# Optimization experiments

Hardware: AMD Instinct MI355X
Metric: run time of the kernel (lower is better)

Reference implementation:

```python
import jax, jax.numpy as jnp
import numpy as np

HEADS = 16
DIM_HEAD = 64


def setup_inputs() -> dict:
    key = jax.random.key(0)
    ks = jax.random.split(key, 5)
    b, n, dim = 4, 2048, 1024
    return {
        "x": jax.random.normal(ks[0], (b, n, dim), dtype=jnp.float32),
        "Wq": jax.random.normal(ks[1], (dim, HEADS * DIM_HEAD), dtype=jnp.float32) * (dim ** -0.5),
        "Wkv": jax.random.normal(ks[2], (dim, DIM_HEAD), dtype=jnp.float32) * (dim ** -0.5),
        "null_kv": jax.random.normal(ks[3], (DIM_HEAD,), dtype=jnp.float32),
        "Wout": jax.random.normal(ks[4], (HEADS * DIM_HEAD, dim), dtype=jnp.float32) * ((HEADS * DIM_HEAD) ** -0.5),
    }


def reference(x, Wq, Wkv, null_kv, Wout):
    b, n, dim = x.shape
    scale = DIM_HEAD ** -0.5
    # q: [b, h, n, d], pre-scaled
    q = (x @ Wq).reshape(b, n, HEADS, DIM_HEAD).transpose(0, 2, 1, 3) * scale
    # shared single-head kv: [b, n, d], prepend null token -> [b, n+1, d]
    kv = x @ Wkv
    kv = jnp.concatenate([jnp.broadcast_to(null_kv, (b, 1, DIM_HEAD)), kv], axis=1)
    # sim: [b, h, n, n+1]
    sim = jnp.einsum('bhid,bjd->bhij', q, kv)
    mask_value = -jnp.finfo(sim.dtype).max
    # causal: query i may attend kv cols 0..i+1 (null at col 0)
    i, j = sim.shape[-2], sim.shape[-1]
    causal_mask = jnp.triu(jnp.ones((i, j), dtype=bool), k=j - i + 1)
    sim = jnp.where(causal_mask, mask_value, sim)
    attn = jax.nn.softmax(sim.astype(jnp.float32), axis=-1)
    out = jnp.einsum('bhij,bjd->bhid', attn, kv.astype(jnp.float32))
    out = out.transpose(0, 2, 1, 3).reshape(b, n, HEADS * DIM_HEAD)
    return out @ Wout
```

## Files before the change

### kernel.cpp

```cpp
#include <hip/hip_runtime.h>
#include <hip/hip_bf16.h>

#define HEADS  16
#define DHEAD  64
#define BATCH  4
#define SEQ    2048
#define DIM    1024
#define KVROWS 2112
#define CSHIFT 24.0f

typedef __hip_bfloat16 bf16;
typedef __attribute__((ext_vector_type(8))) short s8v;
typedef __attribute__((ext_vector_type(4))) short s4v;
typedef __attribute__((ext_vector_type(4))) float f4v;

__device__ __forceinline__ void gl_lds16(const void* g, void* l) {
  __builtin_amdgcn_global_load_lds(
      (const __attribute__((address_space(1))) unsigned int*)g,
      (__attribute__((address_space(3))) unsigned int*)l, 16, 0, 0);
}

__global__ void convert_kernel(const float* __restrict__ in, bf16* __restrict__ out) {
  const size_t i = ((size_t)blockIdx.x * 256 + threadIdx.x) * 8;
  const float4 a = *(const float4*)&in[i];
  const float4 b = *(const float4*)&in[i + 4];
  bf16 v[8] = {__float2bfloat16(a.x), __float2bfloat16(a.y),
               __float2bfloat16(a.z), __float2bfloat16(a.w),
               __float2bfloat16(b.x), __float2bfloat16(b.y),
               __float2bfloat16(b.z), __float2bfloat16(b.w)};
  *(s8v*)&out[i] = *(s8v*)v;
}

__global__ void transpose3_kernel(const float* __restrict__ Wq,
                                  const float* __restrict__ Wout,
                                  const float* __restrict__ Wkv,
                                  bf16* __restrict__ WqkvT,
                                  bf16* __restrict__ WoutT) {
  __shared__ bf16 tile[32][33];
  int bid = blockIdx.x;
  const float* src; bf16* dst; int R, C, bx, by;
  if (bid < 1024)      { src = Wq;   dst = WqkvT;                       R = DIM; C = DIM;   bx = bid & 31; by = bid >> 5; }
  else if (bid < 2048) { bid -= 1024; src = Wout; dst = WoutT;          R = DIM; C = DIM;   bx = bid & 31; by = bid >> 5; }
  else                 { bid -= 2048; src = Wkv;  dst = WqkvT + DIM*DIM; R = DIM; C = DHEAD; bx = bid & 1;  by = bid >> 1; }
  const int c0 = bx * 32, r0 = by * 32;
  const int tx = threadIdx.x, ty = threadIdx.y;
#pragma unroll
  for (int i = 0; i < 32; i += 8)
    tile[ty + i][tx] = __float2bfloat16(src[(size_t)(r0 + ty + i) * C + c0 + tx]);
  __syncthreads();
#pragma unroll
  for (int i = 0; i < 32; i += 8)
    dst[(size_t)(c0 + ty + i) * R + r0 + tx] = tile[tx][ty + i];
}

#define GEMM_CORE(A_, BT_, K_)                                                \
  __shared__ bf16 As[2 * 128 * 64];                                           \
  __shared__ bf16 Bs[2 * 128 * 64];                                           \
  const int m0 = blockIdx.x * 128, n0 = blockIdx.y * 128;                     \
  const int t = threadIdx.x;                                                  \
  const int w = t >> 6, l = t & 63, lr = l & 15, lq = l >> 4;                 \
  const int wm = (w & 1) * 64, wn = (w >> 1) * 64;                            \
  f4v acc[4][4] = {};                                                         \
  const int rowl = l >> 2;                                                    \
  const int cl = ((l & 3) ^ ((l >> 3) & 3)) * 8;                              \
  const bf16* gA0 = (A_)  + (size_t)(m0 + 32 * w + rowl) * (K_) + cl;         \
  const bf16* gA1 = (A_)  + (size_t)(m0 + 32 * w + 16 + rowl) * (K_) + cl;    \
  const bf16* gB0 = (BT_) + (size_t)(n0 + 32 * w + rowl) * (K_) + cl;         \
  const bf16* gB1 = (BT_) + (size_t)(n0 + 32 * w + 16 + rowl) * (K_) + cl;    \
  const int sw = lq ^ ((lr >> 1) & 3);                                        \
  STAGEG(0, 0);                                                               \
  __syncthreads();                                                            \
  int cur = 0;                                                                \
  for (int k0 = 0; k0 < (K_); k0 += 64) {                                     \
    if (k0 + 64 < (K_)) STAGEG(cur ^ 1, k0 + 64);                             \
    const s8v* As16 = (const s8v*)(As + cur * 8192);                          \
    const s8v* Bs16 = (const s8v*)(Bs + cur * 8192);                          \
    _Pragma("unroll")                                                         \
    for (int kw = 0; kw < 2; kw++) {                                          \
      s8v a[4], b[4];                                                         \
      _Pragma("unroll")                                                       \
      for (int mt = 0; mt < 4; mt++)                                          \
        a[mt] = As16[kw * 512 + (wm + mt * 16 + lr) * 4 + sw];                \
      _Pragma("unroll")                                                       \
      for (int ct = 0; ct < 4; ct++)                                          \
        b[ct] = Bs16[kw * 512 + (wn + ct * 16 + lr) * 4 + sw];                \
      _Pragma("unroll")                                                       \
      for (int mt = 0; mt < 4; mt++)                                          \
        _Pragma("unroll")                                                     \
        for (int ct = 0; ct < 4; ct++)                                        \
          acc[mt][ct] = __builtin_amdgcn_mfma_f32_16x16x32_bf16(              \
              a[mt], b[ct], acc[mt][ct], 0, 0, 0);                            \
    }                                                                         \
    __syncthreads();                                                          \
    cur ^= 1;                                                                 \
  }

#define STAGEG(bi, kk)                                                        \
  do {                                                                        \
    gl_lds16(gA0 + (kk),      As + (bi) * 8192 + (2 * w) * 512);              \
    gl_lds16(gA1 + (kk),      As + (bi) * 8192 + (2 * w + 1) * 512);          \
    gl_lds16(gB0 + (kk),      Bs + (bi) * 8192 + (2 * w) * 512);              \
    gl_lds16(gB1 + (kk),      Bs + (bi) * 8192 + (2 * w + 1) * 512);          \
    gl_lds16(gA0 + (kk) + 32, As + (bi) * 8192 + 4096 + (2 * w) * 512);       \
    gl_lds16(gA1 + (kk) + 32, As + (bi) * 8192 + 4096 + (2 * w + 1) * 512);   \
    gl_lds16(gB0 + (kk) + 32, Bs + (bi) * 8192 + 4096 + (2 * w) * 512);       \
    gl_lds16(gB1 + (kk) + 32, Bs + (bi) * 8192 + 4096 + (2 * w + 1) * 512);   \
  } while (0)

__global__ __launch_bounds__(256) void gemm_out_kernel(
    const bf16* __restrict__ A, const bf16* __restrict__ BT,
    float* __restrict__ C, int K) {
  GEMM_CORE(A, BT, K)
#pragma unroll
  for (int mt = 0; mt < 4; mt++)
#pragma unroll
    for (int ct = 0; ct < 4; ct++)
#pragma unroll
      for (int r = 0; r < 4; r++) {
        const int row = m0 + wm + mt * 16 + lq * 4 + r;
        const int col = n0 + wn + ct * 16 + lr;
        C[(size_t)row * DIM + col] = acc[mt][ct][r];
      }
}

__global__ __launch_bounds__(256) void gemm_qkv_kernel(
    const bf16* __restrict__ A, const bf16* __restrict__ BT,
    bf16* __restrict__ q, bf16* __restrict__ kvbuf, bf16* __restrict__ kvbufT,
    int K, float alpha) {
  GEMM_CORE(A, BT, K)
  if (blockIdx.y < 8) {
#pragma unroll
    for (int mt = 0; mt < 4; mt++)
#pragma unroll
      for (int ct = 0; ct < 4; ct++)
#pragma unroll
        for (int r = 0; r < 4; r++) {
          const int row = m0 + wm + mt * 16 + lq * 4 + r;
          const int col = n0 + wn + ct * 16 + lr;
          q[(size_t)row * DIM + col] = __float2bfloat16(acc[mt][ct][r] * alpha);
        }
  } else if (wn == 0) {
#pragma unroll
    for (int mt = 0; mt < 4; mt++)
#pragma unroll
      for (int ct = 0; ct < 4; ct++)
#pragma unroll
        for (int r = 0; r < 4; r++) {
          const int m = m0 + wm + mt * 16 + lq * 4 + r;
          const int c = ct * 16 + lr;
          const int bb = m >> 11, jj = (m & 2047) + 1;
          const bf16 v = __float2bfloat16(acc[mt][ct][r]);
          kvbuf [(size_t)(bb * KVROWS + jj) * DHEAD + c] = v;
          kvbufT[(size_t)(bb * DHEAD + c) * KVROWS + jj] = v;
        }
  }
}

__global__ void fill_null_tail_kernel(const float* __restrict__ null_kv,
                                      bf16* __restrict__ kvbuf,
                                      bf16* __restrict__ kvbufT) {
  const int idx = blockIdx.x * 256 + threadIdx.x;
  const int d = idx & 63;
  const int s = (idx >> 6) & 63;
  const int b = idx >> 12;
  const int row = (s == 0) ? 0 : 2048 + s;
  const bf16 v = (s == 0) ? __float2bfloat16(null_kv[d]) : __float2bfloat16(0.f);
  kvbuf [(size_t)(b * KVROWS + row) * DHEAD + d] = v;
  kvbufT[(size_t)(b * DHEAD + d) * KVROWS + row] = v;
}

__global__ __launch_bounds__(256) void attn_kernel(
    const bf16* __restrict__ q,
    const bf16* __restrict__ kv,
    const bf16* __restrict__ kvT,
    bf16* __restrict__ o) {
  __shared__ bf16 kvs [64][68];
  __shared__ bf16 kvsT[64][68];
  __shared__ bf16 Ps[4][16][68];
  const int t = threadIdx.x, w = t >> 6, l = t & 63, lr = l & 15, lq = l >> 4;
  const int blk = blockIdx.x;
  const int qt = 31 - (blk >> 5);
  const int rem = blk & 31, hp = rem >> 2, b = rem & 3;
  const int q0 = qt * 64;
  const int iw = q0 + w * 16 + lr;

  const bf16* qbase = q + ((size_t)(b * SEQ) + iw) * DIM + hp * 128;
  s8v qb[2][2];
#pragma unroll
  for (int hh = 0; hh < 2; hh++) {
    qb[hh][0] = *(const s8v*)&qbase[hh * 64 + lq * 8];
    qb[hh][1] = *(const s8v*)&qbase[hh * 64 + 32 + lq * 8];
  }

  f4v oaccT[2][4] = {};
  float l_lane[2] = {0.f, 0.f};
  const bf16* kvb  = kv  + (size_t)b * KVROWS * DHEAD;
  const bf16* kvTb = kvT + (size_t)b * DHEAD * KVROWS;
  const int jend = q0 + 65;
  const int srow = t >> 2, scol = (t & 3) * 16;

  s8v rkv0 = *(const s8v*)&kvb[(size_t)srow * DHEAD + scol];
  s8v rkv1 = *(const s8v*)&kvb[(size_t)srow * DHEAD + scol + 8];
  s8v rkT0 = *(const s8v*)&kvTb[(size_t)srow * KVROWS + scol];
  s8v rkT1 = *(const s8v*)&kvTb[(size_t)srow * KVROWS + scol + 8];

  for (int j0 = 0; j0 < jend; j0 += 64) {
    __syncthreads();
    *(s8v*)&kvs[srow][scol]      = rkv0;
    *(s8v*)&kvs[srow][scol + 8]  = rkv1;
    *(s8v*)&kvsT[srow][scol]     = rkT0;
    *(s8v*)&kvsT[srow][scol + 8] = rkT1;
    __syncthreads();

    const int jn = min(j0 + 64, KVROWS - 64);
    rkv0 = *(const s8v*)&kvb[(size_t)(jn + srow) * DHEAD + scol];
    rkv1 = *(const s8v*)&kvb[(size_t)(jn + srow) * DHEAD + scol + 8];
    rkT0 = *(const s8v*)&kvTb[(size_t)srow * KVROWS + jn + scol];
    rkT1 = *(const s8v*)&kvTb[(size_t)srow * KVROWS + jn + scol + 8];

    f4v st[2][4];
#pragma unroll
    for (int jt = 0; jt < 4; jt++) {
      s8v a0 = *(const s8v*)&kvs[jt * 16 + lr][lq * 8];
      s8v a1 = *(const s8v*)&kvs[jt * 16 + lr][32 + lq * 8];
#pragma unroll
      for (int hh = 0; hh < 2; hh++) {
        f4v z = {-CSHIFT, -CSHIFT, -CSHIFT, -CSHIFT};
        z = __builtin_amdgcn_mfma_f32_16x16x32_bf16(a0, qb[hh][0], z, 0, 0, 0);
        z = __builtin_amdgcn_mfma_f32_16x16x32_bf16(a1, qb[hh][1], z, 0, 0, 0);
        st[hh][jt] = z;
      }
    }

    const bool diag = (j0 + 62 > q0 + w * 16);
#pragma unroll
    for (int hh = 0; hh < 2; hh++) {
      if (diag) {
#pragma unroll
        for (int jt = 0; jt < 4; jt++)
#pragma unroll
          for (int r = 0; r < 4; r++) {
            const int jg = j0 + jt * 16 + lq * 4 + r;
            if (jg > iw + 1) st[hh][jt][r] = -1e30f;
          }
      }
      float rs = 0.f;
#pragma unroll
      for (int jt = 0; jt < 4; jt++)
#pragma unroll
        for (int r = 0; r < 4; r++) {
          const float pv = exp2f(st[hh][jt][r]);
          st[hh][jt][r] = pv;
          rs += pv;
        }
      l_lane[hh] += rs;

#pragma unroll
      for (int jt = 0; jt < 4; jt++) {
        s4v pk;
#pragma unroll
        for (int r = 0; r < 4; r++) {
          bf16 h16 = __float2bfloat16(st[hh][jt][r]);
          pk[r] = *(short*)&h16;
        }
        *(s4v*)&Ps[w][lr][jt * 16 + lq * 4] = pk;
      }
      const s8v pb0 = *(const s8v*)&Ps[w][lr][lq * 8];
      const s8v pb1 = *(const s8v*)&Ps[w][lr][32 + lq * 8];
#pragma unroll
      for (int dt = 0; dt < 4; dt++) {
        s8v a0 = *(const s8v*)&kvsT[dt * 16 + lr][lq * 8];
        s8v a1 = *(const s8v*)&kvsT[dt * 16 + lr][32 + lq * 8];
        oaccT[hh][dt] = __builtin_amdgcn_mfma_f32_16x16x32_bf16(a0, pb0, oaccT[hh][dt], 0, 0, 0);
        oaccT[hh][dt] = __builtin_amdgcn_mfma_f32_16x16x32_bf16(a1, pb1, oaccT[hh][dt], 0, 0, 0);
      }
    }
  }

#pragma unroll
  for (int hh = 0; hh < 2; hh++) {
    float lt = l_lane[hh];
    lt += __shfl_xor(lt, 16);
    lt += __shfl_xor(lt, 32);
    const float inv = 1.0f / lt;
#pragma unroll
    for (int dt = 0; dt < 4; dt++) {
      s4v pk;
#pragma unroll
      for (int r = 0; r < 4; r++) {
        bf16 h16 = __float2bfloat16(oaccT[hh][dt][r] * inv);
        pk[r] = *(short*)&h16;
      }
      *(s4v*)&Ps[w][lr][dt * 16 + lq * 4] = pk;
    }
    const int orow = l >> 2, od = (l & 3) * 16;
    s8v o0 = *(const s8v*)&Ps[w][orow][od];
    s8v o1 = *(const s8v*)&Ps[w][orow][od + 8];
    bf16* op = o + ((size_t)(b * SEQ) + q0 + w * 16 + orow) * DIM + hp * 128 + hh * 64 + od;
    *(s8v*)&op[0] = o0;
    *(s8v*)&op[8] = o1;
  }
}

extern "C" void kernel_launch(void* const* d_in, const int* in_sizes, int n_in,
                              void* d_out, int out_size, void* d_ws, size_t ws_size,
                              hipStream_t stream) {
  const float* x       = (const float*)d_in[0];
  const float* Wq      = (const float*)d_in[1];
  const float* Wkv     = (const float*)d_in[2];
  const float* null_kv = (const float*)d_in[3];
  const float* Wout    = (const float*)d_in[4];
  float* out = (float*)d_out;

  char* dob = (char*)d_out;
  bf16* q      = (bf16*)dob;
  bf16* kvbufT = (bf16*)(dob + (size_t)16 * 1024 * 1024);
  char* p = (char*)d_ws;
  bf16* att    = (bf16*)p;
  bf16* xb     = (bf16*)(p + (size_t)16 * 1024 * 1024);
  bf16* WoutT  = (bf16*)(p + (size_t)32 * 1024 * 1024);
  bf16* kvbuf  = (bf16*)(p + (size_t)34 * 1024 * 1024);
  bf16* WqkvT  = att;

  convert_kernel<<<(BATCH * SEQ * DIM) / (256 * 8), 256, 0, stream>>>(x, xb);

  transpose3_kernel<<<2112, dim3(32, 8), 0, stream>>>(Wq, Wout, Wkv, WqkvT, WoutT);

  gemm_qkv_kernel<<<dim3(64, 9), 256, 0, stream>>>(xb, WqkvT, q, kvbuf, kvbufT,
                                                   DIM, 0.125f * 1.44269504089f);
  fill_null_tail_kernel<<<(BATCH * 64 * 64) / 256, 256, 0, stream>>>(null_kv, kvbuf, kvbufT);

  attn_kernel<<<32 * 8 * BATCH, 256, 0, stream>>>(q, kvbuf, kvbufT, att);

  gemm_out_kernel<<<dim3(64, 8), 256, 0, stream>>>(att, WoutT, out, DIM);
}
```

Baseline: 231.6 us.

## Merge prep kernels into one launch and compute softmax row sums via MFMA

Combines the x conversion, weight transposes and null/tail kv fill into a single prep kernel, removing two kernel launches and their gaps. It also moves the fill ahead of the QKV GEMM, which is safe because the rows the fill writes do not overlap the rows the GEMM writes. In the attention kernel, the per-lane exp sum and final cross-lane shuffles are replaced by an MFMA of a ones vector against the bf16 probability tiles. The denominator is then accumulated from the same bf16-rounded P values used for the output, at the cost of two extra MFMAs per block iteration.

```diff
diff --git a/kernel.cpp b/kernel.cpp
--- a/kernel.cpp
+++ b/kernel.cpp
@@ -20,37 +20,50 @@
       (__attribute__((address_space(3))) unsigned int*)l, 16, 0, 0);
 }
 
-__global__ void convert_kernel(const float* __restrict__ in, bf16* __restrict__ out) {
-  const size_t i = ((size_t)blockIdx.x * 256 + threadIdx.x) * 8;
-  const float4 a = *(const float4*)&in[i];
-  const float4 b = *(const float4*)&in[i + 4];
-  bf16 v[8] = {__float2bfloat16(a.x), __float2bfloat16(a.y),
-               __float2bfloat16(a.z), __float2bfloat16(a.w),
-               __float2bfloat16(b.x), __float2bfloat16(b.y),
-               __float2bfloat16(b.z), __float2bfloat16(b.w)};
-  *(s8v*)&out[i] = *(s8v*)v;
-}
-
-__global__ void transpose3_kernel(const float* __restrict__ Wq,
-                                  const float* __restrict__ Wout,
-                                  const float* __restrict__ Wkv,
-                                  bf16* __restrict__ WqkvT,
-                                  bf16* __restrict__ WoutT) {
+__global__ void prep_kernel(const float* __restrict__ x, bf16* __restrict__ xb,
+                            const float* __restrict__ Wq,
+                            const float* __restrict__ Wout,
+                            const float* __restrict__ Wkv,
+                            bf16* __restrict__ WqkvT, bf16* __restrict__ WoutT,
+                            const float* __restrict__ null_kv,
+                            bf16* __restrict__ kvbuf, bf16* __restrict__ kvbufT) {
   __shared__ bf16 tile[32][33];
+  const int t = threadIdx.x;
   int bid = blockIdx.x;
-  const float* src; bf16* dst; int R, C, bx, by;
-  if (bid < 1024)      { src = Wq;   dst = WqkvT;                       R = DIM; C = DIM;   bx = bid & 31; by = bid >> 5; }
-  else if (bid < 2048) { bid -= 1024; src = Wout; dst = WoutT;          R = DIM; C = DIM;   bx = bid & 31; by = bid >> 5; }
-  else                 { bid -= 2048; src = Wkv;  dst = WqkvT + DIM*DIM; R = DIM; C = DHEAD; bx = bid & 1;  by = bid >> 1; }
-  const int c0 = bx * 32, r0 = by * 32;
-  const int tx = threadIdx.x, ty = threadIdx.y;
-#pragma unroll
-  for (int i = 0; i < 32; i += 8)
-    tile[ty + i][tx] = __float2bfloat16(src[(size_t)(r0 + ty + i) * C + c0 + tx]);
-  __syncthreads();
-#pragma unroll
-  for (int i = 0; i < 32; i += 8)
-    dst[(size_t)(c0 + ty + i) * R + r0 + tx] = tile[tx][ty + i];
+  if (bid < 4096) {
+    const size_t i = ((size_t)bid * 256 + t) * 8;
+    const float4 a = *(const float4*)&x[i];
+    const float4 b = *(const float4*)&x[i + 4];
+    bf16 v[8] = {__float2bfloat16(a.x), __float2bfloat16(a.y),
+                 __float2bfloat16(a.z), __float2bfloat16(a.w),
+                 __float2bfloat16(b.x), __float2bfloat16(b.y),
+                 __float2bfloat16(b.z), __float2bfloat16(b.w)};
+    *(s8v*)&xb[i] = *(s8v*)v;
+  } else if (bid < 6208) {
+    bid -= 4096;
+    const float* src; bf16* dst; int C, bx, by;
+    if (bid < 1024)      { src = Wq;   dst = WqkvT;             C = DIM;   bx = bid & 31; by = bid >> 5; }
+    else if (bid < 2048) { bid -= 1024; src = Wout; dst = WoutT; C = DIM;  bx = bid & 31; by = bid >> 5; }
+    else                 { bid -= 2048; src = Wkv;  dst = WqkvT + DIM * DIM; C = DHEAD; bx = bid & 1; by = bid >> 1; }
+    const int c0 = bx * 32, r0 = by * 32;
+    const int tx = t & 31, ty = t >> 5;
+#pragma unroll
+    for (int i = 0; i < 32; i += 8)
+      tile[ty + i][tx] = __float2bfloat16(src[(size_t)(r0 + ty + i) * C + c0 + tx]);
+    __syncthreads();
+#pragma unroll
+    for (int i = 0; i < 32; i += 8)
+      dst[(size_t)(c0 + ty + i) * DIM + r0 + tx] = tile[tx][ty + i];
+  } else {
+    const int idx = (bid - 6208) * 256 + t;
+    const int d = idx & 63;
+    const int s = (idx >> 6) & 63;
+    const int b = idx >> 12;
+    const int row = (s == 0) ? 0 : 2048 + s;
+    const bf16 v = (s == 0) ? __float2bfloat16(null_kv[d]) : __float2bfloat16(0.f);
+    kvbuf [(size_t)(b * KVROWS + row) * DHEAD + d] = v;
+    kvbufT[(size_t)(b * DHEAD + d) * KVROWS + row] = v;
+  }
 }
 
 #define GEMM_CORE(A_, BT_, K_)                                                \
@@ -156,19 +169,6 @@
   }
 }
 
-__global__ void fill_null_tail_kernel(const float* __restrict__ null_kv,
-                                      bf16* __restrict__ kvbuf,
-                                      bf16* __restrict__ kvbufT) {
-  const int idx = blockIdx.x * 256 + threadIdx.x;
-  const int d = idx & 63;
-  const int s = (idx >> 6) & 63;
-  const int b = idx >> 12;
-  const int row = (s == 0) ? 0 : 2048 + s;
-  const bf16 v = (s == 0) ? __float2bfloat16(null_kv[d]) : __float2bfloat16(0.f);
-  kvbuf [(size_t)(b * KVROWS + row) * DHEAD + d] = v;
-  kvbufT[(size_t)(b * DHEAD + d) * KVROWS + row] = v;
-}
-
 __global__ __launch_bounds__(256) void attn_kernel(
     const bf16* __restrict__ q,
     const bf16* __restrict__ kv,
@@ -193,7 +193,10 @@
   }
 
   f4v oaccT[2][4] = {};
-  float l_lane[2] = {0.f, 0.f};
+  f4v lacc[2] = {};
+  const short onebf = (short)0x3F80;
+  const s8v ones = {onebf, onebf, onebf, onebf, onebf, onebf, onebf, onebf};
+
   const bf16* kvb  = kv  + (size_t)b * KVROWS * DHEAD;
   const bf16* kvTb = kvT + (size_t)b * DHEAD * KVROWS;
   const int jend = q0 + 65;
@@ -244,16 +247,11 @@
             if (jg > iw + 1) st[hh][jt][r] = -1e30f;
           }
       }
-      float rs = 0.f;
 #pragma unroll
       for (int jt = 0; jt < 4; jt++)
 #pragma unroll
-        for (int r = 0; r < 4; r++) {
-          const float pv = exp2f(st[hh][jt][r]);
-          st[hh][jt][r] = pv;
-          rs += pv;
-        }
-      l_lane[hh] += rs;
+        for (int r = 0; r < 4; r++)
+          st[hh][jt][r] = exp2f(st[hh][jt][r]);
 
 #pragma unroll
       for (int jt = 0; jt < 4; jt++) {
@@ -267,6 +265,10 @@
       }
       const s8v pb0 = *(const s8v*)&Ps[w][lr][lq * 8];
       const s8v pb1 = *(const s8v*)&Ps[w][lr][32 + lq * 8];
+
+      lacc[hh] = __builtin_amdgcn_mfma_f32_16x16x32_bf16(ones, pb0, lacc[hh], 0, 0, 0);
+      lacc[hh] = __builtin_amdgcn_mfma_f32_16x16x32_bf16(ones, pb1, lacc[hh], 0, 0, 0);
+
 #pragma unroll
       for (int dt = 0; dt < 4; dt++) {
         s8v a0 = *(const s8v*)&kvsT[dt * 16 + lr][lq * 8];
@@ -279,10 +281,7 @@
 
 #pragma unroll
   for (int hh = 0; hh < 2; hh++) {
-    float lt = l_lane[hh];
-    lt += __shfl_xor(lt, 16);
-    lt += __shfl_xor(lt, 32);
-    const float inv = 1.0f / lt;
+    const float inv = 1.0f / lacc[hh][0];
 #pragma unroll
     for (int dt = 0; dt < 4; dt++) {
       s4v pk;
@@ -322,13 +321,11 @@
   bf16* kvbuf  = (bf16*)(p + (size_t)34 * 1024 * 1024);
   bf16* WqkvT  = att;
 
-  convert_kernel<<<(BATCH * SEQ * DIM) / (256 * 8), 256, 0, stream>>>(x, xb);
-
-  transpose3_kernel<<<2112, dim3(32, 8), 0, stream>>>(Wq, Wout, Wkv, WqkvT, WoutT);
+  prep_kernel<<<6272, 256, 0, stream>>>(x, xb, Wq, Wout, Wkv, WqkvT, WoutT,
+                                        null_kv, kvbuf, kvbufT);
 
   gemm_qkv_kernel<<<dim3(64, 9), 256, 0, stream>>>(xb, WqkvT, q, kvbuf, kvbufT,
                                                    DIM, 0.125f * 1.44269504089f);
-  fill_null_tail_kernel<<<(BATCH * 64 * 64) / 256, 256, 0, stream>>>(null_kv, kvbuf, kvbufT);
 
   attn_kernel<<<32 * 8 * BATCH, 256, 0, stream>>>(q, kvbuf, kvbufT, att);
 
```

New measurement: 229.3 us. No clear change (-1.0%).
